# Performance work log

Hardware: AMD Instinct MI355X
Metric: run time of the kernel (lower is better)

The kernel has to match this reference:

```python
import jax, jax.numpy as jnp
import numpy as np

NA = 131072
DG = 150          # GRU hidden size
DS = 50           # static context dim
DIN = 12          # decoding_steps * 2
VEL_CONST = 0.5


def setup_inputs() -> dict:
    key = jax.random.key(0)
    ks = jax.random.split(key, 18)
    s = 0.1  # weight init scale keeps exp(apd_2) numerically tame
    inp = {
        "z": jax.random.normal(ks[0], (NA, 2), jnp.float32),
        "x_flat": jax.random.normal(ks[1], (NA, DIN), jnp.float32),
        "h": jax.random.normal(ks[2], (1, NA, DG), jnp.float32),
        "static": jax.random.normal(ks[3], (NA, DS), jnp.float32),
        "dx": jax.random.normal(ks[4], (NA, 2), jnp.float32),
        "x_prev": jax.random.normal(ks[5], (NA, 2), jnp.float32),
        # GRU params (torch layout: gates ordered r, z, n; shape [3*DG, in])
        "W_ih": jax.random.normal(ks[6], (3 * DG, DIN), jnp.float32) * s,
        "W_hh": jax.random.normal(ks[7], (3 * DG, DG), jnp.float32) * s,
        "b_ih": jax.random.normal(ks[8], (3 * DG,), jnp.float32) * s,
        "b_hh": jax.random.normal(ks[9], (3 * DG,), jnp.float32) * s,
        # MLP: Linear(200,50) -> Softplus -> Linear(50,50) -> Tanh -> Linear(50,6)
        "W1": jax.random.normal(ks[10], (50, DG + DS), jnp.float32) * s,
        "b1": jax.random.normal(ks[11], (50,), jnp.float32) * s,
        "W2": jax.random.normal(ks[12], (50, 50), jnp.float32) * s,
        "b2": jax.random.normal(ks[13], (50,), jnp.float32) * s,
        "W3": jax.random.normal(ks[14], (6, 50), jnp.float32) * s,
        "b3": jax.random.normal(ks[15], (6,), jnp.float32) * s,
    }
    return inp


def _gru_cell(x, h0, W_ih, W_hh, b_ih, b_hh):
    # torch GRU single step. x: [Na, DIN], h0: [Na, DG]
    gx = x @ W_ih.T + b_ih          # [Na, 3*DG]
    gh = h0 @ W_hh.T + b_hh         # [Na, 3*DG]
    xr, xz, xn = jnp.split(gx, 3, axis=-1)
    hr, hz, hn = jnp.split(gh, 3, axis=-1)
    r = jax.nn.sigmoid(xr + hr)
    zg = jax.nn.sigmoid(xz + hz)
    n = jnp.tanh(xn + r * hn)
    return (1.0 - zg) * n + zg * h0


def reference(z, x_flat, h, static, dx, x_prev,
              W_ih, W_hh, b_ih, b_hh, W1, b1, W2, b2, W3, b3):
    h_new = _gru_cell(x_flat, h[0], W_ih, W_hh, b_ih, b_hh)  # [Na, DG]
    dyn_static = jnp.concatenate([h_new, static], axis=-1)    # [Na, DG+DS]
    hmlp = jax.nn.softplus(dyn_static @ W1.T + b1)
    hmlp = jnp.tanh(hmlp @ W2.T + b2)
    out = hmlp @ W3.T + b3                                    # [Na, 6]

    mu_hat = out[:, :2]
    sh = out[:, 2:].reshape(-1, 2, 2)                         # sigma_hat
    mu = x_prev + VEL_CONST * dx + mu_hat

    b = sh[:, 0, 1] + sh[:, 1, 0]
    apd_2 = sh[:, 0, 0] + sh[:, 1, 1]
    amd_2 = sh[:, 0, 0] - sh[:, 1, 1]
    delta = jnp.sqrt(amd_2 ** 2 + b ** 2)
    sinh = jnp.sinh(delta)
    cosh = jnp.cosh(delta)
    tmp1 = sinh / delta
    tmp2 = amd_2 / tmp1
    s00 = cosh + tmp2
    s01 = b * tmp1
    s11 = cosh - tmp2
    sigma = jnp.stack([jnp.stack([s00, s01], axis=-1),
                       jnp.stack([s01, s11], axis=-1)], axis=-2)  # [Na,2,2]
    sigma = sigma * jnp.exp(apd_2)[:, None, None]

    x = jnp.einsum('nij,nj->ni', sigma, z) + mu
    return x, mu, sigma, h_new[None]
```

## Files before the change

kernel.cpp:

```cpp
#include <hip/hip_runtime.h>
#include <math.h>

#define NA 131072
#define NBLK128 (NA/128)

typedef __bf16 bf16x8 __attribute__((ext_vector_type(8)));
typedef float f32x16 __attribute__((ext_vector_type(16)));

#define APACK_OFF 0
#define BIAS4_OFF 214016
#define W1P_OFF   216448
#define W2P_OFF   243072

__device__ __forceinline__ unsigned short f2b(float f){
  __bf16 h = (__bf16)f;
  unsigned short u;
  __builtin_memcpy(&u, &h, 2);
  return u;
}
__device__ __forceinline__ float b2f(unsigned short u){
  unsigned x = ((unsigned)u) << 16; float f;
  __builtin_memcpy(&f, &x, 4); return f;
}
__device__ __forceinline__ bf16x8 asb(uint4 u){ return __builtin_bit_cast(bf16x8, u); }
__device__ __forceinline__ f32x16 mfma32(bf16x8 a, bf16x8 b, f32x16 c){
  return __builtin_amdgcn_mfma_f32_32x32x16_bf16(a, b, c, 0, 0, 0);
}
__device__ __forceinline__ float fsigmoid(float x){ return 1.f/(1.f+__expf(-x)); }
__device__ __forceinline__ float ftanh(float x){ return 1.f - 2.f/(__expf(2.f*x)+1.f); }

__global__ __launch_bounds__(256) void prep2(
    const float* __restrict__ W_ih, const float* __restrict__ W_hh,
    const float* __restrict__ b_ih, const float* __restrict__ b_hh,
    const float* __restrict__ W1, const float* __restrict__ W2,
    float* __restrict__ ws)
{
  int tid = blockIdx.x*blockDim.x + threadIdx.x;
  int stride = gridDim.x*blockDim.x;
  unsigned short* Ap  = (unsigned short*)((char*)ws + APACK_OFF);
  float*          B4  = (float*)((char*)ws + BIAS4_OFF);
  unsigned short* W1p = (unsigned short*)((char*)ws + W1P_OFF);
  unsigned short* W2p = (unsigned short*)((char*)ws + W2P_OFF);

  for (int s = tid; s < 19*11*64; s += stride){
    int lane = s & 63; int t2 = s >> 6; int ks = t2 % 11; int mt = t2 / 11;
    int R = mt*32 + (lane & 31);
    int kb = ks*16 + (lane >> 5)*8;
    int j = R >> 2, g = R & 3;
    #pragma unroll
    for (int i=0;i<8;i++){
      int k = kb + i; float f = 0.f;
      if (j < 150){
        if (k < 12){
          if (g==0) f = W_ih[j*12+k];
          else if (g==1) f = W_ih[(150+j)*12+k];
          else if (g==3) f = W_ih[(300+j)*12+k];
        } else if (k >= 16 && k < 166){
          int kh = k - 16;
          if (g==0) f = W_hh[j*150+kh];
          else if (g==1) f = W_hh[(150+j)*150+kh];
          else if (g==2) f = W_hh[(300+j)*150+kh];
        }
      }
      Ap[s*8+i] = f2b(f);
    }
  }
  for (int j = tid; j < 152; j += stride){
    float4 bv = make_float4(0.f,0.f,0.f,0.f);
    if (j < 150){
      bv.x = b_ih[j]       + b_hh[j];
      bv.y = b_ih[150+j]   + b_hh[150+j];
      bv.z = b_hh[300+j];
      bv.w = b_ih[300+j];
    }
    ((float4*)B4)[j] = bv;
  }
  for (int s = tid; s < 2*13*64; s += stride){
    int lane = s & 63; int t2 = s >> 6; int ks = t2 % 13; int mt = t2 / 13;
    int o = mt*32 + (lane & 31);
    int kb = ks*16 + (lane >> 5)*8;
    #pragma unroll
    for (int i=0;i<8;i++){
      int k = kb + i;
      float f = (o < 50 && k < 200) ? W1[o*200+k] : 0.f;
      W1p[s*8+i] = f2b(f);
    }
  }
  for (int s = tid; s < 2*4*64; s += stride){
    int lane = s & 63; int t2 = s >> 6; int ks = t2 % 4; int mt = t2 / 4;
    int o = mt*32 + (lane & 31);
    int kb = ks*16 + (lane >> 5)*8;
    #pragma unroll
    for (int i=0;i<8;i++){
      int k = kb + i;
      float f = (o < 50 && k < 50) ? W2[o*50+k] : 0.f;
      W2p[s*8+i] = f2b(f);
    }
  }
}

__global__ __launch_bounds__(512,4) void fused_kernel(
    const float* __restrict__ x_flat, const float* __restrict__ h_in,
    const float* __restrict__ st, const float* __restrict__ z_in,
    const float* __restrict__ dx, const float* __restrict__ xp,
    const float* __restrict__ b1, const float* __restrict__ b2,
    const float* __restrict__ W3, const float* __restrict__ b3,
    const unsigned short* __restrict__ Apack, const float* __restrict__ Bias4,
    const unsigned short* __restrict__ W1p, const unsigned short* __restrict__ W2p,
    float* __restrict__ out)
{
  __shared__ char smem[73728];
  unsigned short* sm_ag = (unsigned short*)smem;
  unsigned short* sm_xf = (unsigned short*)(smem + 55296);
  unsigned short* sm_h1 = (unsigned short*)(smem + 55296);
  float*          sm_h2 = (float*)smem;
  unsigned*       ag32  = (unsigned*)sm_ag;

  int t = threadIdx.x; int lane = t & 63; int w = t >> 6;
  int hi = lane >> 5, cl = lane & 31;
  int nt = w & 3;
  int mlane = w >> 2;
  long ab = (long)blockIdx.x * 128;

  const float2* h2p = (const float2*)h_in;
  for (int s = t; s < 9600; s += 512){
    int a = s/75, k2 = s - a*75;
    float2 v = h2p[ab*75 + s];
    ag32[a*108 + k2] = (unsigned)f2b(v.x) | ((unsigned)f2b(v.y) << 16);
  }
  const float2* s2p = (const float2*)st;
  for (int s = t; s < 3200; s += 512){
    int a = s/25, k2 = s - a*25;
    float2 v = s2p[ab*25 + s];
    ag32[a*108 + 75 + k2] = (unsigned)f2b(v.x) | ((unsigned)f2b(v.y) << 16);
  }
  for (int s = t; s < 1024; s += 512)
    ag32[(s>>3)*108 + 100 + (s&7)] = 0u;
  for (int s = t; s < 2048; s += 512){
    int nt2 = s >> 9; int r = s & 511; int ln = r >> 3; int i = r & 7;
    int k = ((ln >> 5) << 3) + i;
    int agent = nt2*32 + (ln & 31);
    unsigned short v = 0;
    if (k < 12) v = f2b(x_flat[(ab+agent)*12 + k]);
    sm_xf[s] = v;
  }
  __syncthreads();

  const uint4* xfv = (const uint4*)sm_xf;
  const uint4* r0v = (const uint4*)(sm_ag + (nt*32 + cl)*216);
  bf16x8 B0[11];
  B0[0] = asb(xfv[nt*64 + lane]);
  #pragma unroll
  for (int ks=1; ks<11; ks++) B0[ks] = asb(r0v[(ks-1)*2 + hi]);
  __syncthreads();

  for (int s = t; s < 4608; s += 512) ((unsigned*)sm_h1)[s] = 0u;

  const uint4* ApV = (const uint4*)Apack;
  #pragma unroll 1
  for (int mt = mlane; mt < 19; mt += 2){
    f32x16 acc0;
    #pragma unroll
    for (int q=0;q<4;q++){
      float4 bq = ((const float4*)Bias4)[mt*8 + 2*q + hi];
      acc0[4*q+0]=bq.x; acc0[4*q+1]=bq.y; acc0[4*q+2]=bq.z; acc0[4*q+3]=bq.w;
    }
    const uint4* ap = ApV + (size_t)(mt*11)*64 + lane;
    #pragma unroll
    for (int ks=0; ks<11; ks++){
      acc0 = mfma32(asb(ap[ks*64]), B0[ks], acc0);
    }
    int a = nt*32 + cl;
    #pragma unroll
    for (int q=0;q<4;q++){
      int j = mt*8 + 2*q + hi;
      if (j < 150){
        float h0 = b2f(sm_ag[a*216 + j]);
        float r = fsigmoid(acc0[4*q+0]);
        float z = fsigmoid(acc0[4*q+1]);
        float n = ftanh(acc0[4*q+3] + r*acc0[4*q+2]);
        sm_ag[a*216 + j] = f2b(n + z*(h0 - n));
      }
    }
  }
  __syncthreads();

  float2* oh2 = (float2*)(out + (size_t)8*NA);
  for (int s = t; s < 9600; s += 512){
    unsigned u = ag32[(s/75)*108 + (s - (s/75)*75)];
    float2 v; v.x = b2f((unsigned short)u); v.y = b2f((unsigned short)(u>>16));
    oh2[ab*75 + s] = v;
  }

  int mt2 = mlane; int a2 = nt*32 + cl;
  {
    f32x16 acc;
    #pragma unroll
    for (int r=0;r<16;r++){
      int o = mt2*32 + (r&3) + 8*(r>>2) + 4*hi;
      acc[r] = (o < 50) ? b1[o] : 0.f;
    }
    {
      const uint4* rv  = (const uint4*)(sm_ag + a2*216);
      const uint4* w1v = (const uint4*)W1p;
      #pragma unroll
      for (int ks=0; ks<13; ks++){
        acc = mfma32(asb(w1v[(mt2*13+ks)*64 + lane]), asb(rv[ks*2+hi]), acc);
      }
    }
    #pragma unroll
    for (int r=0;r<16;r++){
      int o = mt2*32 + (r&3) + 8*(r>>2) + 4*hi;
      if (o < 50){
        float xx = acc[r];
        float spv = fmaxf(xx,0.f) + __logf(1.f + __expf(-fabsf(xx)));
        sm_h1[a2*72 + o] = f2b(spv);
      }
    }
  }
  __syncthreads();

  {
    f32x16 acc2;
    #pragma unroll
    for (int r=0;r<16;r++){
      int o = mt2*32 + (r&3) + 8*(r>>2) + 4*hi;
      acc2[r] = (o < 50) ? b2[o] : 0.f;
    }
    {
      const uint4* r1v = (const uint4*)(sm_h1 + a2*72);
      const uint4* w2v = (const uint4*)W2p;
      #pragma unroll
      for (int ks=0; ks<4; ks++){
        acc2 = mfma32(asb(w2v[(mt2*4+ks)*64 + lane]), asb(r1v[ks*2+hi]), acc2);
      }
    }
    #pragma unroll
    for (int r=0;r<16;r++){
      int o = mt2*32 + (r&3) + 8*(r>>2) + 4*hi;
      if (o < 50) sm_h2[a2*51 + o] = ftanh(acc2[r]);
    }
  }
  __syncthreads();

  if (t < 128){
    int a = t; long ga = ab + a;
    float o6[6];
    #pragma unroll
    for (int jj=0;jj<6;jj++) o6[jj] = b3[jj];
    for (int k=0;k<50;k++){
      float v = sm_h2[a*51 + k];
      #pragma unroll
      for (int jj=0;jj<6;jj++) o6[jj] = fmaf(v, W3[jj*50+k], o6[jj]);
    }
    float mu0 = xp[ga*2+0] + 0.5f*dx[ga*2+0] + o6[0];
    float mu1 = xp[ga*2+1] + 0.5f*dx[ga*2+1] + o6[1];
    float bb  = o6[3] + o6[4];
    float apd = o6[2] + o6[5];
    float amd = o6[2] - o6[5];
    float delta = sqrtf(amd*amd + bb*bb);
    float e  = __expf(delta);
    float ei = 1.f/e;
    float sinh_ = 0.5f*(e - ei);
    float cosh_ = 0.5f*(e + ei);
    float tmp1 = sinh_/delta;
    float tmp2 = amd/tmp1;
    float ea = __expf(apd);
    float s00 = (cosh_+tmp2)*ea;
    float s01 = (bb*tmp1)*ea;
    float s11 = (cosh_-tmp2)*ea;
    float z0 = z_in[ga*2+0], z1 = z_in[ga*2+1];
    out[ga*2+0] = s00*z0 + s01*z1 + mu0;
    out[ga*2+1] = s01*z0 + s11*z1 + mu1;
    out[(size_t)2*NA + ga*2+0] = mu0;
    out[(size_t)2*NA + ga*2+1] = mu1;
    out[(size_t)4*NA + ga*4+0] = s00;
    out[(size_t)4*NA + ga*4+1] = s01;
    out[(size_t)4*NA + ga*4+2] = s01;
    out[(size_t)4*NA + ga*4+3] = s11;
  }
}

extern "C" void kernel_launch(void* const* d_in, const int* in_sizes, int n_in,
                              void* d_out, int out_size, void* d_ws, size_t ws_size,
                              hipStream_t stream) {
  const float* z      = (const float*)d_in[0];
  const float* x_flat = (const float*)d_in[1];
  const float* h      = (const float*)d_in[2];
  const float* st     = (const float*)d_in[3];
  const float* dx     = (const float*)d_in[4];
  const float* xp     = (const float*)d_in[5];
  const float* W_ih   = (const float*)d_in[6];
  const float* W_hh   = (const float*)d_in[7];
  const float* b_ih   = (const float*)d_in[8];
  const float* b_hh   = (const float*)d_in[9];
  const float* W1     = (const float*)d_in[10];
  const float* b1     = (const float*)d_in[11];
  const float* W2     = (const float*)d_in[12];
  const float* b2     = (const float*)d_in[13];
  const float* W3     = (const float*)d_in[14];
  const float* b3     = (const float*)d_in[15];
  float* out = (float*)d_out;
  float* ws  = (float*)d_ws;

  const unsigned short* Apack = (const unsigned short*)((char*)ws + APACK_OFF);
  const float*          Bias4 = (const float*)((char*)ws + BIAS4_OFF);
  const unsigned short* W1p   = (const unsigned short*)((char*)ws + W1P_OFF);
  const unsigned short* W2p   = (const unsigned short*)((char*)ws + W2P_OFF);

  hipLaunchKernelGGL(prep2, dim3(128), dim3(256), 0, stream,
                     W_ih, W_hh, b_ih, b_hh, W1, W2, ws);
  hipLaunchKernelGGL(fused_kernel, dim3(NBLK128), dim3(512), 0, stream,
                     x_flat, h, st, z, dx, xp, b1, b2, W3, b3,
                     Apack, Bias4, W1p, W2p, out);
}
```

Before: 110.8 us.

## Switch to 16x16x32 MFMA tiles with 64-agent blocks and compact shared layout

Result: slower. 133.0 us (+20.1%).

```diff
diff --git a/kernel.cpp b/kernel.cpp
--- a/kernel.cpp
+++ b/kernel.cpp
@@ -2,15 +2,15 @@
 #include <math.h>
 
 #define NA 131072
-#define NBLK128 (NA/128)
+#define NBLK64 (NA/64)
 
 typedef __bf16 bf16x8 __attribute__((ext_vector_type(8)));
-typedef float f32x16 __attribute__((ext_vector_type(16)));
+typedef float f32x4 __attribute__((ext_vector_type(4)));
 
 #define APACK_OFF 0
-#define BIAS4_OFF 214016
-#define W1P_OFF   216448
-#define W2P_OFF   243072
+#define BIAS4_OFF 233472
+#define W1P_OFF   235904
+#define W2P_OFF   264576
 
 __device__ __forceinline__ unsigned short f2b(float f){
   __bf16 h = (__bf16)f;
@@ -23,8 +23,8 @@
   __builtin_memcpy(&f, &x, 4); return f;
 }
 __device__ __forceinline__ bf16x8 asb(uint4 u){ return __builtin_bit_cast(bf16x8, u); }
-__device__ __forceinline__ f32x16 mfma32(bf16x8 a, bf16x8 b, f32x16 c){
-  return __builtin_amdgcn_mfma_f32_32x32x16_bf16(a, b, c, 0, 0, 0);
+__device__ __forceinline__ f32x4 mfma16(bf16x8 a, bf16x8 b, f32x4 c){
+  return __builtin_amdgcn_mfma_f32_16x16x32_bf16(a, b, c, 0, 0, 0);
 }
 __device__ __forceinline__ float fsigmoid(float x){ return 1.f/(1.f+__expf(-x)); }
 __device__ __forceinline__ float ftanh(float x){ return 1.f - 2.f/(__expf(2.f*x)+1.f); }
@@ -42,10 +42,10 @@
   unsigned short* W1p = (unsigned short*)((char*)ws + W1P_OFF);
   unsigned short* W2p = (unsigned short*)((char*)ws + W2P_OFF);
 
-  for (int s = tid; s < 19*11*64; s += stride){
-    int lane = s & 63; int t2 = s >> 6; int ks = t2 % 11; int mt = t2 / 11;
-    int R = mt*32 + (lane & 31);
-    int kb = ks*16 + (lane >> 5)*8;
+  for (int s = tid; s < 38*6*64; s += stride){
+    int lane = s & 63; int t2 = s >> 6; int ks = t2 % 6; int mt = t2 / 6;
+    int R = mt*16 + (lane & 15);
+    int kb = ks*32 + (lane >> 4)*8;
     int j = R >> 2, g = R & 3;
     #pragma unroll
     for (int i=0;i<8;i++){
@@ -75,21 +75,25 @@
     }
     ((float4*)B4)[j] = bv;
   }
-  for (int s = tid; s < 2*13*64; s += stride){
-    int lane = s & 63; int t2 = s >> 6; int ks = t2 % 13; int mt = t2 / 13;
-    int o = mt*32 + (lane & 31);
-    int kb = ks*16 + (lane >> 5)*8;
+  for (int s = tid; s < 4*7*64; s += stride){
+    int lane = s & 63; int t2 = s >> 6; int ks = t2 % 7; int mt = t2 / 7;
+    int o = mt*16 + (lane & 15);
+    int kb = ks*32 + (lane >> 4)*8;
     #pragma unroll
     for (int i=0;i<8;i++){
       int k = kb + i;
-      float f = (o < 50 && k < 200) ? W1[o*200+k] : 0.f;
+      float f = 0.f;
+      if (o < 50){
+        if (k >= 16 && k < 166) f = W1[o*200 + (k-16)];
+        else if (k >= 166 && k < 216) f = W1[o*200 + 150 + (k-166)];
+      }
       W1p[s*8+i] = f2b(f);
     }
   }
-  for (int s = tid; s < 2*4*64; s += stride){
-    int lane = s & 63; int t2 = s >> 6; int ks = t2 % 4; int mt = t2 / 4;
-    int o = mt*32 + (lane & 31);
-    int kb = ks*16 + (lane >> 5)*8;
+  for (int s = tid; s < 4*2*64; s += stride){
+    int lane = s & 63; int t2 = s >> 6; int ks = t2 % 2; int mt = t2 / 2;
+    int o = mt*16 + (lane & 15);
+    int kb = ks*32 + (lane >> 4)*8;
     #pragma unroll
     for (int i=0;i<8;i++){
       int k = kb + i;
@@ -99,155 +103,140 @@
   }
 }
 
-__global__ __launch_bounds__(512,4) void fused_kernel(
+__global__ __launch_bounds__(512,8) void fused_kernel(
     const float* __restrict__ x_flat, const float* __restrict__ h_in,
     const float* __restrict__ st, const float* __restrict__ z_in,
     const float* __restrict__ dx, const float* __restrict__ xp,
-    const float* __restrict__ b1, const float* __restrict__ b2,
-    const float* __restrict__ W3, const float* __restrict__ b3,
+    const float* __restrict__ pb1, const float* __restrict__ pb2,
+    const float* __restrict__ W3, const float* __restrict__ pb3,
     const unsigned short* __restrict__ Apack, const float* __restrict__ Bias4,
     const unsigned short* __restrict__ W1p, const unsigned short* __restrict__ W2p,
     float* __restrict__ out)
 {
-  __shared__ char smem[73728];
+  __shared__ char smem[38912];
   unsigned short* sm_ag = (unsigned short*)smem;
-  unsigned short* sm_xf = (unsigned short*)(smem + 55296);
-  unsigned short* sm_h1 = (unsigned short*)(smem + 55296);
+  unsigned short* sm_h1 = (unsigned short*)(smem + 29696);
   float*          sm_h2 = (float*)smem;
   unsigned*       ag32  = (unsigned*)sm_ag;
+  unsigned*       h1w   = (unsigned*)sm_h1;
 
   int t = threadIdx.x; int lane = t & 63; int w = t >> 6;
-  int hi = lane >> 5, cl = lane & 31;
-  int nt = w & 3;
-  int mlane = w >> 2;
-  long ab = (long)blockIdx.x * 128;
+  int q4 = lane >> 4, c16 = lane & 15;
+  int nt = w & 3, mpar = w >> 2;
+  int agent = nt*16 + c16;
+  long ab = (long)blockIdx.x * 64;
 
   const float2* h2p = (const float2*)h_in;
-  for (int s = t; s < 9600; s += 512){
+  for (int s = t; s < 4800; s += 512){
     int a = s/75, k2 = s - a*75;
     float2 v = h2p[ab*75 + s];
-    ag32[a*108 + k2] = (unsigned)f2b(v.x) | ((unsigned)f2b(v.y) << 16);
+    ag32[a*116 + 8 + k2] = (unsigned)f2b(v.x) | ((unsigned)f2b(v.y) << 16);
   }
   const float2* s2p = (const float2*)st;
-  for (int s = t; s < 3200; s += 512){
+  for (int s = t; s < 1600; s += 512){
     int a = s/25, k2 = s - a*25;
     float2 v = s2p[ab*25 + s];
-    ag32[a*108 + 75 + k2] = (unsigned)f2b(v.x) | ((unsigned)f2b(v.y) << 16);
-  }
-  for (int s = t; s < 1024; s += 512)
-    ag32[(s>>3)*108 + 100 + (s&7)] = 0u;
-  for (int s = t; s < 2048; s += 512){
-    int nt2 = s >> 9; int r = s & 511; int ln = r >> 3; int i = r & 7;
-    int k = ((ln >> 5) << 3) + i;
-    int agent = nt2*32 + (ln & 31);
-    unsigned short v = 0;
-    if (k < 12) v = f2b(x_flat[(ab+agent)*12 + k]);
-    sm_xf[s] = v;
-  }
-  __syncthreads();
-
-  const uint4* xfv = (const uint4*)sm_xf;
-  const uint4* r0v = (const uint4*)(sm_ag + (nt*32 + cl)*216);
-  bf16x8 B0[11];
-  B0[0] = asb(xfv[nt*64 + lane]);
+    ag32[a*116 + 83 + k2] = (unsigned)f2b(v.x) | ((unsigned)f2b(v.y) << 16);
+  }
+  const float2* x2p = (const float2*)x_flat;
+  for (int s = t; s < 384; s += 512){
+    int a = s/6, p = s - a*6;
+    float2 v = x2p[ab*6 + s];
+    ag32[a*116 + p] = (unsigned)f2b(v.x) | ((unsigned)f2b(v.y) << 16);
+  }
+  for (int s = t; s < 640; s += 512){
+    int a = s/10, q = s - a*10;
+    int idx = (q < 2) ? (6 + q) : (106 + q);
+    ag32[a*116 + idx] = 0u;
+  }
+  for (int s = t; s < 2304; s += 512) h1w[s] = 0u;
+  __syncthreads();
+
+  const uint4* rv = (const uint4*)(sm_ag + agent*232);
+  bf16x8 B0[6];
   #pragma unroll
-  for (int ks=1; ks<11; ks++) B0[ks] = asb(r0v[(ks-1)*2 + hi]);
-  __syncthreads();
-
-  for (int s = t; s < 4608; s += 512) ((unsigned*)sm_h1)[s] = 0u;
+  for (int ks=0; ks<6; ks++) B0[ks] = asb(rv[ks*4 + q4]);
+  __syncthreads();
 
   const uint4* ApV = (const uint4*)Apack;
   #pragma unroll 1
-  for (int mt = mlane; mt < 19; mt += 2){
-    f32x16 acc0;
-    #pragma unroll
-    for (int q=0;q<4;q++){
-      float4 bq = ((const float4*)Bias4)[mt*8 + 2*q + hi];
-      acc0[4*q+0]=bq.x; acc0[4*q+1]=bq.y; acc0[4*q+2]=bq.z; acc0[4*q+3]=bq.w;
-    }
-    const uint4* ap = ApV + (size_t)(mt*11)*64 + lane;
-    #pragma unroll
-    for (int ks=0; ks<11; ks++){
-      acc0 = mfma32(asb(ap[ks*64]), B0[ks], acc0);
-    }
-    int a = nt*32 + cl;
-    #pragma unroll
-    for (int q=0;q<4;q++){
-      int j = mt*8 + 2*q + hi;
-      if (j < 150){
-        float h0 = b2f(sm_ag[a*216 + j]);
-        float r = fsigmoid(acc0[4*q+0]);
-        float z = fsigmoid(acc0[4*q+1]);
-        float n = ftanh(acc0[4*q+3] + r*acc0[4*q+2]);
-        sm_ag[a*216 + j] = f2b(n + z*(h0 - n));
-      }
+  for (int mt = mpar; mt < 38; mt += 2){
+    float4 bq = ((const float4*)Bias4)[mt*4 + q4];
+    f32x4 acc; acc[0]=bq.x; acc[1]=bq.y; acc[2]=bq.z; acc[3]=bq.w;
+    const uint4* ap = ApV + (size_t)(mt*6)*64 + lane;
+    #pragma unroll
+    for (int ks=0; ks<6; ks++) acc = mfma16(asb(ap[ks*64]), B0[ks], acc);
+    int j = mt*4 + q4;
+    if (j < 150){
+      float h0 = b2f(sm_ag[agent*232 + 16 + j]);
+      float r = fsigmoid(acc[0]);
+      float z = fsigmoid(acc[1]);
+      float n = ftanh(acc[3] + r*acc[2]);
+      sm_ag[agent*232 + 16 + j] = f2b(n + z*(h0 - n));
     }
   }
   __syncthreads();
 
   float2* oh2 = (float2*)(out + (size_t)8*NA);
-  for (int s = t; s < 9600; s += 512){
-    unsigned u = ag32[(s/75)*108 + (s - (s/75)*75)];
+  for (int s = t; s < 4800; s += 512){
+    int a = s/75, k2 = s - a*75;
+    unsigned u = ag32[a*116 + 8 + k2];
     float2 v; v.x = b2f((unsigned short)u); v.y = b2f((unsigned short)(u>>16));
     oh2[ab*75 + s] = v;
   }
 
-  int mt2 = mlane; int a2 = nt*32 + cl;
-  {
-    f32x16 acc;
-    #pragma unroll
-    for (int r=0;r<16;r++){
-      int o = mt2*32 + (r&3) + 8*(r>>2) + 4*hi;
-      acc[r] = (o < 50) ? b1[o] : 0.f;
-    }
-    {
-      const uint4* rv  = (const uint4*)(sm_ag + a2*216);
-      const uint4* w1v = (const uint4*)W1p;
-      #pragma unroll
-      for (int ks=0; ks<13; ks++){
-        acc = mfma32(asb(w1v[(mt2*13+ks)*64 + lane]), asb(rv[ks*2+hi]), acc);
-      }
-    }
-    #pragma unroll
-    for (int r=0;r<16;r++){
-      int o = mt2*32 + (r&3) + 8*(r>>2) + 4*hi;
+  const uint4* w1v = (const uint4*)W1p;
+  #pragma unroll
+  for (int s2 = 0; s2 < 2; s2++){
+    int mt1 = mpar*2 + s2;
+    f32x4 acc;
+    #pragma unroll
+    for (int r=0;r<4;r++){
+      int o = mt1*16 + q4*4 + r;
+      acc[r] = (o < 50) ? pb1[o] : 0.f;
+    }
+    #pragma unroll
+    for (int ks=0; ks<7; ks++)
+      acc = mfma16(asb(w1v[(mt1*7+ks)*64 + lane]), asb(rv[ks*4 + q4]), acc);
+    #pragma unroll
+    for (int r=0;r<4;r++){
+      int o = mt1*16 + q4*4 + r;
       if (o < 50){
         float xx = acc[r];
         float spv = fmaxf(xx,0.f) + __logf(1.f + __expf(-fabsf(xx)));
-        sm_h1[a2*72 + o] = f2b(spv);
+        sm_h1[agent*72 + o] = f2b(spv);
       }
     }
   }
   __syncthreads();
 
-  {
-    f32x16 acc2;
-    #pragma unroll
-    for (int r=0;r<16;r++){
-      int o = mt2*32 + (r&3) + 8*(r>>2) + 4*hi;
-      acc2[r] = (o < 50) ? b2[o] : 0.f;
-    }
-    {
-      const uint4* r1v = (const uint4*)(sm_h1 + a2*72);
-      const uint4* w2v = (const uint4*)W2p;
-      #pragma unroll
-      for (int ks=0; ks<4; ks++){
-        acc2 = mfma32(asb(w2v[(mt2*4+ks)*64 + lane]), asb(r1v[ks*2+hi]), acc2);
-      }
-    }
-    #pragma unroll
-    for (int r=0;r<16;r++){
-      int o = mt2*32 + (r&3) + 8*(r>>2) + 4*hi;
-      if (o < 50) sm_h2[a2*51 + o] = ftanh(acc2[r]);
-    }
-  }
-  __syncthreads();
-
-  if (t < 128){
+  const uint4* w2v = (const uint4*)W2p;
+  const uint4* h1v = (const uint4*)(sm_h1 + agent*72);
+  #pragma unroll
+  for (int s2 = 0; s2 < 2; s2++){
+    int mt1 = mpar*2 + s2;
+    f32x4 acc2;
+    #pragma unroll
+    for (int r=0;r<4;r++){
+      int o = mt1*16 + q4*4 + r;
+      acc2[r] = (o < 50) ? pb2[o] : 0.f;
+    }
+    #pragma unroll
+    for (int ks=0; ks<2; ks++)
+      acc2 = mfma16(asb(w2v[(mt1*2+ks)*64 + lane]), asb(h1v[ks*4 + q4]), acc2);
+    #pragma unroll
+    for (int r=0;r<4;r++){
+      int o = mt1*16 + q4*4 + r;
+      if (o < 50) sm_h2[agent*51 + o] = ftanh(acc2[r]);
+    }
+  }
+  __syncthreads();
+
+  if (t < 64){
     int a = t; long ga = ab + a;
     float o6[6];
     #pragma unroll
-    for (int jj=0;jj<6;jj++) o6[jj] = b3[jj];
+    for (int jj=0;jj<6;jj++) o6[jj] = pb3[jj];
     for (int k=0;k<50;k++){
       float v = sm_h2[a*51 + k];
       #pragma unroll
@@ -310,7 +299,7 @@
 
   hipLaunchKernelGGL(prep2, dim3(128), dim3(256), 0, stream,
                      W_ih, W_hh, b_ih, b_hh, W1, W2, ws);
-  hipLaunchKernelGGL(fused_kernel, dim3(NBLK128), dim3(512), 0, stream,
+  hipLaunchKernelGGL(fused_kernel, dim3(NBLK64), dim3(512), 0, stream,
                      x_flat, h, st, z, dx, xp, b1, b2, W3, b3,
                      Apack, Bias4, W1p, W2p, out);
 }
```
